# Optimization experiments

Hardware: AMD Instinct MI355X
Metric: run time of the kernel (lower is better)

## Reference

```python
import jax, jax.numpy as jnp
import numpy as np

D_IN = 1024
D_OUT = 1024
N_HEADS = 16
HEAD_DIM = D_IN // N_HEADS      # 64
HEAD_DIM_V = D_OUT // N_HEADS   # 64


def setup_inputs() -> dict:
    key = jax.random.key(0)
    ks = jax.random.split(key, 7)
    s = 0.02
    x = jax.random.normal(ks[0], (4, 2048, D_IN), dtype=jnp.float32)
    Wq = jax.random.normal(ks[1], (D_IN, D_IN), dtype=jnp.float32) * s
    bq = jnp.zeros((D_IN,), dtype=jnp.float32)
    Wk = jax.random.normal(ks[2], (D_IN, D_IN), dtype=jnp.float32) * s
    bk = jnp.zeros((D_IN,), dtype=jnp.float32)
    Wv = jax.random.normal(ks[3], (D_IN, D_OUT), dtype=jnp.float32) * s
    bv = jnp.zeros((D_OUT,), dtype=jnp.float32)
    return {"x": x, "Wq": Wq, "bq": bq, "Wk": Wk, "bk": bk, "Wv": Wv, "bv": bv}


def reference(x, Wq, bq, Wk, bk, Wv, bv):
    B, S, _ = x.shape
    scale = jnp.sqrt(jnp.asarray(HEAD_DIM, dtype=jnp.float32))
    # projections -> [B, S, H, Dh] -> [B, H, S, Dh]
    q = (x @ Wq + bq).reshape(B, S, N_HEADS, HEAD_DIM).transpose(0, 2, 1, 3)
    k = (x @ Wk + bk).reshape(B, S, N_HEADS, HEAD_DIM).transpose(0, 2, 1, 3)
    v = (x @ Wv + bv).reshape(B, S, N_HEADS, HEAD_DIM_V).transpose(0, 2, 1, 3)
    # [B, H, S, S] attention scores (naive full materialization, as in source)
    scores = jnp.einsum("bhsd,bhtd->bhst", q, k) / scale
    weights = jax.nn.softmax(scores, axis=-1)
    out = jnp.einsum("bhst,bhtd->bhsd", weights, v)
    # [B, H, S, Dv] -> [B, S, H*Dv]  (out_projection NOT applied in source forward)
    return out.transpose(0, 2, 1, 3).reshape(B, S, N_HEADS * HEAD_DIM_V)
```

## Files before the change

kernel.cpp:

```cpp
#include <hip/hip_runtime.h>

#define B_  4
#define S_  2048
#define D_  1024
#define H_  16
#define DH_ 64
#define M_  (B_ * S_)

typedef __attribute__((ext_vector_type(8))) short short8;
typedef __attribute__((ext_vector_type(4))) float floatx4;

__device__ __forceinline__ float bf2f(unsigned short u) {
    union { unsigned int i; float f; } v; v.i = ((unsigned int)u) << 16; return v.f;
}
__device__ __forceinline__ unsigned short f2bf(float f) {
    union { float f; unsigned int i; } v; v.f = f;
    unsigned int r = v.i + 0x7fffu + ((v.i >> 16) & 1u);
    return (unsigned short)(r >> 16);
}
__device__ __forceinline__ unsigned int pk_trunc(float a, float b) {
    return (__float_as_uint(a) >> 16) | (__float_as_uint(b) & 0xffff0000u);
}

typedef const __attribute__((address_space(1))) unsigned int* gas_ptr;
typedef __attribute__((address_space(3))) unsigned int* las_ptr;
__device__ __forceinline__ void async_cp16(const void* g, void* l) {
    __builtin_amdgcn_global_load_lds((gas_ptr)g, (las_ptr)l, 16, 0, 0);
}

__global__ __launch_bounds__(256) void cast_x_kernel(
    const float* __restrict__ x, unsigned short* __restrict__ Ax)
{
    int i4 = blockIdx.x * 256 + threadIdx.x;
    float4 v = reinterpret_cast<const float4*>(x)[i4];
    ushort4 o;
    o.x = f2bf(v.x); o.y = f2bf(v.y); o.z = f2bf(v.z); o.w = f2bf(v.w);
    reinterpret_cast<ushort4*>(Ax)[i4] = o;
}

__global__ __launch_bounds__(256) void cast_w_T_kernel(
    const float* __restrict__ W, unsigned short* __restrict__ Wt)
{
    __shared__ unsigned short T[64][72];
    const int t = threadIdx.x;
    const int k0 = blockIdx.x * 64, n0 = blockIdx.y * 64;

    #pragma unroll
    for (int p = 0; p < 4; ++p) {
        int kr = p * 16 + (t >> 4);
        int nc = (t & 15) * 4;
        float4 v = *reinterpret_cast<const float4*>(W + (size_t)(k0 + kr) * D_ + n0 + nc);
        T[nc + 0][kr] = f2bf(v.x);
        T[nc + 1][kr] = f2bf(v.y);
        T[nc + 2][kr] = f2bf(v.z);
        T[nc + 3][kr] = f2bf(v.w);
    }
    __syncthreads();

    const int nl = t >> 2, kc = (t & 3) * 16;
    size_t base = (size_t)(n0 + nl) * D_ + k0 + kc;
    *reinterpret_cast<short8*>(Wt + base)     = *reinterpret_cast<const short8*>(&T[nl][kc]);
    *reinterpret_cast<short8*>(Wt + base + 8) = *reinterpret_cast<const short8*>(&T[nl][kc + 8]);
}

__global__ __launch_bounds__(256) void gemm_qkv_mfma(
    const unsigned short* __restrict__ Ax,
    const unsigned short* __restrict__ Wtq,
    const unsigned short* __restrict__ Wtk,
    const unsigned short* __restrict__ Wtv,
    const float* __restrict__ bq, const float* __restrict__ bk,
    const float* __restrict__ bv,
    unsigned short* __restrict__ Q, unsigned short* __restrict__ K,
    unsigned short* __restrict__ Vtg)
{
    __shared__ unsigned short As[128 * 32];
    __shared__ unsigned short Bs[128 * 32];

    const int tid = threadIdx.x;
    const int lane = tid & 63;
    const int w = tid >> 6;
    const int wm = (w >> 1) * 64, wn = (w & 1) * 64;
    const int l15 = lane & 15, quad = lane >> 4;

    const int hw   = blockIdx.x;
    const int xcd  = hw & 7;
    const int slot = hw >> 3;
    const int gcol = slot >> 3;
    const int mi   = slot & 7;
    const int m0   = (xcd * 8 + mi) * 128;
    const int n0   = (gcol & 7) * 128;
    const int mat  = gcol >> 3;

    const unsigned short* Wt = mat == 0 ? Wtq : (mat == 1 ? Wtk : Wtv);
    const float* bias        = mat == 0 ? bq  : (mat == 1 ? bk  : bv);

    const int arow = tid >> 2;
    const int acol = (tid & 3) * 8;

    floatx4 acc[4][4] = {};

    for (int kb = 0; kb < 32; ++kb) {
        int cb = kb * 32;
        __syncthreads();
        async_cp16(Ax + (size_t)(m0 + arow) * D_ + cb + acol,      As + arow * 32 + acol);
        async_cp16(Ax + (size_t)(m0 + 64 + arow) * D_ + cb + acol, As + (64 + arow) * 32 + acol);
        async_cp16(Wt + (size_t)(n0 + arow) * D_ + cb + acol,      Bs + arow * 32 + acol);
        async_cp16(Wt + (size_t)(n0 + 64 + arow) * D_ + cb + acol, Bs + (64 + arow) * 32 + acol);
        __syncthreads();

        short8 af[4], bf[4];
        #pragma unroll
        for (int i = 0; i < 4; ++i)
            af[i] = *reinterpret_cast<const short8*>(As + (wm + i * 16 + l15) * 32 + quad * 8);
        #pragma unroll
        for (int j = 0; j < 4; ++j)
            bf[j] = *reinterpret_cast<const short8*>(Bs + (wn + j * 16 + l15) * 32 + quad * 8);
        #pragma unroll
        for (int i = 0; i < 4; ++i)
            #pragma unroll
            for (int j = 0; j < 4; ++j)
                acc[i][j] = __builtin_amdgcn_mfma_f32_16x16x32_bf16(af[i], bf[j], acc[i][j], 0, 0, 0);
    }

    float bb[4];
    #pragma unroll
    for (int j = 0; j < 4; ++j) bb[j] = bias[n0 + wn + j * 16 + l15];

    if (mat == 2) {
        const int b = m0 >> 11;
        #pragma unroll
        for (int i = 0; i < 4; ++i) {
            int srow = (m0 & 2047) + wm + i * 16 + quad * 4;
            #pragma unroll
            for (int j = 0; j < 4; ++j) {
                int col = n0 + wn + j * 16 + l15;
                ushort4 o;
                o.x = f2bf(acc[i][j][0] + bb[j]);
                o.y = f2bf(acc[i][j][1] + bb[j]);
                o.z = f2bf(acc[i][j][2] + bb[j]);
                o.w = f2bf(acc[i][j][3] + bb[j]);
                *reinterpret_cast<ushort4*>(Vtg + (size_t)(b * 1024 + col) * S_ + srow) = o;
            }
        }
    } else {
        unsigned short* C = (mat == 0) ? Q : K;
        const float sc = (mat == 0) ? 0.125f : 1.0f;
        #pragma unroll
        for (int i = 0; i < 4; ++i)
            #pragma unroll
            for (int r = 0; r < 4; ++r) {
                int row = m0 + wm + i * 16 + quad * 4 + r;
                #pragma unroll
                for (int j = 0; j < 4; ++j)
                    C[(size_t)row * D_ + n0 + wn + j * 16 + l15] = f2bf((acc[i][j][r] + bb[j]) * sc);
            }
    }
}

#define KT_   64
#define PITCH 72

__global__ __launch_bounds__(256, 4) void attn_mfma(
    const unsigned short* __restrict__ Qg,
    const unsigned short* __restrict__ Kg,
    const unsigned short* __restrict__ Vtg,
    float* __restrict__ out)
{
    __shared__ unsigned short Ks[KT_ * PITCH];
    __shared__ unsigned short Vt[DH_ * PITCH];

    const int tid  = threadIdx.x;
    const int wq   = tid >> 6;
    const int lane = tid & 63;
    const int l15  = lane & 15;
    const int quad = lane >> 4;

    const int id  = blockIdx.x;
    const int bh  = (id & 7) * 8 + ((id >> 3) & 7);
    const int qt  = id >> 6;
    const int b   = bh >> 4;
    const int colbase = (bh & 15) * DH_;
    const int rowQ0 = b * S_ + qt * 128;

    short8 qf[2][2];
    #pragma unroll
    for (int g = 0; g < 2; ++g) {
        int qrow = rowQ0 + wq * 32 + g * 16 + l15;
        qf[g][0] = *reinterpret_cast<const short8*>(Qg + (size_t)qrow * D_ + colbase + quad * 8);
        qf[g][1] = *reinterpret_cast<const short8*>(Qg + (size_t)qrow * D_ + colbase + 32 + quad * 8);
    }

    floatx4 Oacc[2][4] = {};
    float lsum[2] = {0.f, 0.f};

    const int srow = tid >> 3;
    const int sc8  = (tid & 7) * 8;
    const int vc  = sc8 >> 4;
    const int vqk = (sc8 >> 2) & 3;
    const int vk0 = ((vc & 1) << 2) + ((vc >> 1) << 5) + (vqk << 3);

    const unsigned short* Kbase = Kg + (size_t)(b * S_) * D_ + colbase;
    const unsigned short* Vbase = Vtg + (size_t)(bh * 64) * S_;

    short8 kpre[2], vpre[2];
    #pragma unroll
    for (int p = 0; p < 2; ++p) {
        kpre[p] = *reinterpret_cast<const short8*>(Kbase + (size_t)(p * 32 + srow) * D_ + sc8);
        vpre[p] = *reinterpret_cast<const short8*>(Vbase + (size_t)(p * 32 + srow) * S_ + sc8);
    }

    for (int kt = 0; kt < S_ / KT_; ++kt) {
        __syncthreads();
        #pragma unroll
        for (int p = 0; p < 2; ++p) {
            *reinterpret_cast<short8*>(&Ks[(p * 32 + srow) * PITCH + sc8]) = kpre[p];
            uint4 u = __builtin_bit_cast(uint4, vpre[p]);
            uint2 lo, hi;
            lo.x = u.x; lo.y = u.y; hi.x = u.z; hi.y = u.w;
            *reinterpret_cast<uint2*>(&Vt[(p * 32 + srow) * PITCH + vk0])     = lo;
            *reinterpret_cast<uint2*>(&Vt[(p * 32 + srow) * PITCH + vk0 + 8]) = hi;
        }
        if (kt + 1 < S_ / KT_) {
            int off = (kt + 1) * KT_;
            #pragma unroll
            for (int p = 0; p < 2; ++p) {
                kpre[p] = *reinterpret_cast<const short8*>(Kbase + (size_t)(off + p * 32 + srow) * D_ + sc8);
                vpre[p] = *reinterpret_cast<const short8*>(Vbase + (size_t)(p * 32 + srow) * S_ + off + sc8);
            }
        }
        __syncthreads();

        #pragma unroll
        for (int half = 0; half < 2; ++half) {
            floatx4 s_[2][2];
            #pragma unroll
            for (int ci = 0; ci < 2; ++ci) {
                int c = half * 2 + ci;
                short8 kf0 = *reinterpret_cast<const short8*>(&Ks[(c * 16 + l15) * PITCH + quad * 8]);
                short8 kf1 = *reinterpret_cast<const short8*>(&Ks[(c * 16 + l15) * PITCH + 32 + quad * 8]);
                #pragma unroll
                for (int g = 0; g < 2; ++g) {
                    floatx4 a = {0.f, 0.f, 0.f, 0.f};
                    a = __builtin_amdgcn_mfma_f32_16x16x32_bf16(kf0, qf[g][0], a, 0, 0, 0);
                    a = __builtin_amdgcn_mfma_f32_16x16x32_bf16(kf1, qf[g][1], a, 0, 0, 0);
                    s_[g][ci] = a;
                }
            }
            short8 pa[2];
            #pragma unroll
            for (int g = 0; g < 2; ++g) {
                float p00 = __expf(s_[g][0][0]), p01 = __expf(s_[g][0][1]);
                float p02 = __expf(s_[g][0][2]), p03 = __expf(s_[g][0][3]);
                float p10 = __expf(s_[g][1][0]), p11 = __expf(s_[g][1][1]);
                float p12 = __expf(s_[g][1][2]), p13 = __expf(s_[g][1][3]);
                lsum[g] += (p00 + p01) + (p02 + p03) + (p10 + p11) + (p12 + p13);
                uint4 pu;
                pu.x = pk_trunc(p00, p01);
                pu.y = pk_trunc(p02, p03);
                pu.z = pk_trunc(p10, p11);
                pu.w = pk_trunc(p12, p13);
                pa[g] = __builtin_bit_cast(short8, pu);
            }
            #pragma unroll
            for (int d = 0; d < 4; ++d) {
                short8 vf = *reinterpret_cast<const short8*>(
                    &Vt[(d * 16 + l15) * PITCH + half * 32 + quad * 8]);
                #pragma unroll
                for (int g = 0; g < 2; ++g)
                    Oacc[g][d] = __builtin_amdgcn_mfma_f32_16x16x32_bf16(pa[g], vf, Oacc[g][d], 0, 0, 0);
            }
        }
    }

    #pragma unroll
    for (int g = 0; g < 2; ++g) {
        float lred = lsum[g];
        lred += __shfl_xor(lred, 16);
        lred += __shfl_xor(lred, 32);
        float inv[4];
        #pragma unroll
        for (int r = 0; r < 4; ++r)
            inv[r] = 1.f / __shfl(lred, quad * 4 + r);
        int orow = rowQ0 + wq * 32 + g * 16 + quad * 4;
        #pragma unroll
        for (int r = 0; r < 4; ++r)
            #pragma unroll
            for (int d = 0; d < 4; ++d)
                out[(size_t)(orow + r) * D_ + colbase + d * 16 + l15] = Oacc[g][d][r] * inv[r];
    }
}

extern "C" void kernel_launch(void* const* d_in, const int* in_sizes, int n_in,
                              void* d_out, int out_size, void* d_ws, size_t ws_size,
                              hipStream_t stream) {
    const float* x  = (const float*)d_in[0];
    const float* Wq = (const float*)d_in[1];
    const float* bq = (const float*)d_in[2];
    const float* Wk = (const float*)d_in[3];
    const float* bk = (const float*)d_in[4];
    const float* Wv = (const float*)d_in[5];
    const float* bv = (const float*)d_in[6];
    float* out = (float*)d_out;

    unsigned short* Q   = (unsigned short*)d_ws;
    unsigned short* K   = Q + (size_t)M_ * D_;
    unsigned short* Vtg = K + (size_t)M_ * D_;
    unsigned short* Ax  = Vtg + (size_t)M_ * D_;
    unsigned short* Wtq = Ax + (size_t)M_ * D_;
    unsigned short* Wtk = Wtq + (size_t)D_ * D_;
    unsigned short* Wtv = Wtk + (size_t)D_ * D_;

    cast_x_kernel<<<M_ * D_ / 4 / 256, 256, 0, stream>>>(x, Ax);
    dim3 gw(16, 16);
    cast_w_T_kernel<<<gw, 256, 0, stream>>>(Wq, Wtq);
    cast_w_T_kernel<<<gw, 256, 0, stream>>>(Wk, Wtk);
    cast_w_T_kernel<<<gw, 256, 0, stream>>>(Wv, Wtv);

    gemm_qkv_mfma<<<1536, 256, 0, stream>>>(Ax, Wtq, Wtk, Wtv, bq, bk, bv, Q, K, Vtg);

    attn_mfma<<<1024, 256, 0, stream>>>(Q, K, Vtg, out);
}
```

Measured before the change: 257.8 us.

## Halve attention query tile, fold log2e into Q scale, merge weight casts

The attention kernel now gives each block 64 query rows (16 per wave) instead of 128 and launches twice as many blocks, with a launch bound that allows 8 blocks per CU for higher occupancy. The log2(e) factor is folded into the Q scaling so softmax uses a native exp2, and bf16 packing uses a byte-permute instruction. The three weight cast/transpose launches become one 3D-grid launch. The trade-off is that each K/V tile staged in LDS is reused by half as many query rows, which doubles K/V global traffic and LDS staging work per output.

Measured after the change: 296.4 us. +15.0%, slower.

```diff
diff --git a/kernel.cpp b/kernel.cpp
--- a/kernel.cpp
+++ b/kernel.cpp
@@ -19,8 +19,18 @@
     return (unsigned short)(r >> 16);
 }
 __device__ __forceinline__ unsigned int pk_trunc(float a, float b) {
+#if __has_builtin(__builtin_amdgcn_perm)
+    return __builtin_amdgcn_perm(__float_as_uint(b), __float_as_uint(a), 0x07060302u);
+#else
     return (__float_as_uint(a) >> 16) | (__float_as_uint(b) & 0xffff0000u);
-}
+#endif
+}
+
+#if __has_builtin(__builtin_amdgcn_exp2f)
+#define EXP2(x) __builtin_amdgcn_exp2f(x)
+#else
+#define EXP2(x) __expf(0.6931471805599453f * (x))
+#endif
 
 typedef const __attribute__((address_space(1))) unsigned int* gas_ptr;
 typedef __attribute__((address_space(3))) unsigned int* las_ptr;
@@ -39,8 +49,14 @@
 }
 
 __global__ __launch_bounds__(256) void cast_w_T_kernel(
-    const float* __restrict__ W, unsigned short* __restrict__ Wt)
+    const float* __restrict__ W0, const float* __restrict__ W1,
+    const float* __restrict__ W2,
+    unsigned short* __restrict__ T0, unsigned short* __restrict__ T1,
+    unsigned short* __restrict__ T2)
 {
+    const float* W = blockIdx.z == 0 ? W0 : (blockIdx.z == 1 ? W1 : W2);
+    unsigned short* Wt = blockIdx.z == 0 ? T0 : (blockIdx.z == 1 ? T1 : T2);
+
     __shared__ unsigned short T[64][72];
     const int t = threadIdx.x;
     const int k0 = blockIdx.x * 64, n0 = blockIdx.y * 64;
@@ -144,7 +160,7 @@
         }
     } else {
         unsigned short* C = (mat == 0) ? Q : K;
-        const float sc = (mat == 0) ? 0.125f : 1.0f;
+        const float sc = (mat == 0) ? 0.18033688011112042f : 1.0f;
         #pragma unroll
         for (int i = 0; i < 4; ++i)
             #pragma unroll
@@ -160,7 +176,7 @@
 #define KT_   64
 #define PITCH 72
 
-__global__ __launch_bounds__(256, 4) void attn_mfma(
+__global__ __launch_bounds__(256, 8) void attn_mfma(
     const unsigned short* __restrict__ Qg,
     const unsigned short* __restrict__ Kg,
     const unsigned short* __restrict__ Vtg,
@@ -180,18 +196,17 @@
     const int qt  = id >> 6;
     const int b   = bh >> 4;
     const int colbase = (bh & 15) * DH_;
-    const int rowQ0 = b * S_ + qt * 128;
-
-    short8 qf[2][2];
-    #pragma unroll
-    for (int g = 0; g < 2; ++g) {
-        int qrow = rowQ0 + wq * 32 + g * 16 + l15;
-        qf[g][0] = *reinterpret_cast<const short8*>(Qg + (size_t)qrow * D_ + colbase + quad * 8);
-        qf[g][1] = *reinterpret_cast<const short8*>(Qg + (size_t)qrow * D_ + colbase + 32 + quad * 8);
-    }
-
-    floatx4 Oacc[2][4] = {};
-    float lsum[2] = {0.f, 0.f};
+    const int rowQ0 = b * S_ + qt * 64;
+
+    short8 qf[2];
+    {
+        int qrow = rowQ0 + wq * 16 + l15;
+        qf[0] = *reinterpret_cast<const short8*>(Qg + (size_t)qrow * D_ + colbase + quad * 8);
+        qf[1] = *reinterpret_cast<const short8*>(Qg + (size_t)qrow * D_ + colbase + 32 + quad * 8);
+    }
+
+    floatx4 Oacc[4] = {};
+    float lsum = 0.f;
 
     const int srow = tid >> 3;
     const int sc8  = (tid & 7) * 8;
@@ -232,62 +247,50 @@
 
         #pragma unroll
         for (int half = 0; half < 2; ++half) {
-            floatx4 s_[2][2];
+            floatx4 s_[2];
             #pragma unroll
             for (int ci = 0; ci < 2; ++ci) {
                 int c = half * 2 + ci;
                 short8 kf0 = *reinterpret_cast<const short8*>(&Ks[(c * 16 + l15) * PITCH + quad * 8]);
                 short8 kf1 = *reinterpret_cast<const short8*>(&Ks[(c * 16 + l15) * PITCH + 32 + quad * 8]);
-                #pragma unroll
-                for (int g = 0; g < 2; ++g) {
-                    floatx4 a = {0.f, 0.f, 0.f, 0.f};
-                    a = __builtin_amdgcn_mfma_f32_16x16x32_bf16(kf0, qf[g][0], a, 0, 0, 0);
-                    a = __builtin_amdgcn_mfma_f32_16x16x32_bf16(kf1, qf[g][1], a, 0, 0, 0);
-                    s_[g][ci] = a;
-                }
-            }
-            short8 pa[2];
-            #pragma unroll
-            for (int g = 0; g < 2; ++g) {
-                float p00 = __expf(s_[g][0][0]), p01 = __expf(s_[g][0][1]);
-                float p02 = __expf(s_[g][0][2]), p03 = __expf(s_[g][0][3]);
-                float p10 = __expf(s_[g][1][0]), p11 = __expf(s_[g][1][1]);
-                float p12 = __expf(s_[g][1][2]), p13 = __expf(s_[g][1][3]);
-                lsum[g] += (p00 + p01) + (p02 + p03) + (p10 + p11) + (p12 + p13);
-                uint4 pu;
-                pu.x = pk_trunc(p00, p01);
-                pu.y = pk_trunc(p02, p03);
-                pu.z = pk_trunc(p10, p11);
-                pu.w = pk_trunc(p12, p13);
-                pa[g] = __builtin_bit_cast(short8, pu);
-            }
+                floatx4 a = {0.f, 0.f, 0.f, 0.f};
+                a = __builtin_amdgcn_mfma_f32_16x16x32_bf16(kf0, qf[0], a, 0, 0, 0);
+                a = __builtin_amdgcn_mfma_f32_16x16x32_bf16(kf1, qf[1], a, 0, 0, 0);
+                s_[ci] = a;
+            }
+            float p00 = EXP2(s_[0][0]), p01 = EXP2(s_[0][1]);
+            float p02 = EXP2(s_[0][2]), p03 = EXP2(s_[0][3]);
+            float p10 = EXP2(s_[1][0]), p11 = EXP2(s_[1][1]);
+            float p12 = EXP2(s_[1][2]), p13 = EXP2(s_[1][3]);
+            lsum += (p00 + p01) + (p02 + p03) + (p10 + p11) + (p12 + p13);
+            uint4 pu;
+            pu.x = pk_trunc(p00, p01);
+            pu.y = pk_trunc(p02, p03);
+            pu.z = pk_trunc(p10, p11);
+            pu.w = pk_trunc(p12, p13);
+            short8 pa = __builtin_bit_cast(short8, pu);
             #pragma unroll
             for (int d = 0; d < 4; ++d) {
                 short8 vf = *reinterpret_cast<const short8*>(
                     &Vt[(d * 16 + l15) * PITCH + half * 32 + quad * 8]);
-                #pragma unroll
-                for (int g = 0; g < 2; ++g)
-                    Oacc[g][d] = __builtin_amdgcn_mfma_f32_16x16x32_bf16(pa[g], vf, Oacc[g][d], 0, 0, 0);
+                Oacc[d] = __builtin_amdgcn_mfma_f32_16x16x32_bf16(pa, vf, Oacc[d], 0, 0, 0);
             }
         }
     }
 
-    #pragma unroll
-    for (int g = 0; g < 2; ++g) {
-        float lred = lsum[g];
-        lred += __shfl_xor(lred, 16);
-        lred += __shfl_xor(lred, 32);
-        float inv[4];
-        #pragma unroll
-        for (int r = 0; r < 4; ++r)
-            inv[r] = 1.f / __shfl(lred, quad * 4 + r);
-        int orow = rowQ0 + wq * 32 + g * 16 + quad * 4;
-        #pragma unroll
-        for (int r = 0; r < 4; ++r)
-            #pragma unroll
-            for (int d = 0; d < 4; ++d)
-                out[(size_t)(orow + r) * D_ + colbase + d * 16 + l15] = Oacc[g][d][r] * inv[r];
-    }
+    float lred = lsum;
+    lred += __shfl_xor(lred, 16);
+    lred += __shfl_xor(lred, 32);
+    float inv[4];
+    #pragma unroll
+    for (int r = 0; r < 4; ++r)
+        inv[r] = 1.f / __shfl(lred, quad * 4 + r);
+    int orow = rowQ0 + wq * 16 + quad * 4;
+    #pragma unroll
+    for (int r = 0; r < 4; ++r)
+        #pragma unroll
+        for (int d = 0; d < 4; ++d)
+            out[(size_t)(orow + r) * D_ + colbase + d * 16 + l15] = Oacc[d][r] * inv[r];
 }
 
 extern "C" void kernel_launch(void* const* d_in, const int* in_sizes, int n_in,
@@ -311,12 +314,10 @@
     unsigned short* Wtv = Wtk + (size_t)D_ * D_;
 
     cast_x_kernel<<<M_ * D_ / 4 / 256, 256, 0, stream>>>(x, Ax);
-    dim3 gw(16, 16);
-    cast_w_T_kernel<<<gw, 256, 0, stream>>>(Wq, Wtq);
-    cast_w_T_kernel<<<gw, 256, 0, stream>>>(Wk, Wtk);
-    cast_w_T_kernel<<<gw, 256, 0, stream>>>(Wv, Wtv);
+    dim3 gw(16, 16, 3);
+    cast_w_T_kernel<<<gw, 256, 0, stream>>>(Wq, Wk, Wv, Wtq, Wtk, Wtv);
 
     gemm_qkv_mfma<<<1536, 256, 0, stream>>>(Ax, Wtq, Wtk, Wtv, bq, bk, bv, Q, K, Vtg);
 
-    attn_mfma<<<1024, 256, 0, stream>>>(Q, K, Vtg, out);
-}
+    attn_mfma<<<2048, 256, 0, stream>>>(Q, K, Vtg, out);
+}
```
